# Performance work log

Hardware: AMD Instinct MI355X
Metric: run time of the kernel (lower is better)

## Reference

```python
import jax, jax.numpy as jnp
import numpy as np

IMAGE_SIZE = 224
BLUR_SIGMA = 4.0  # PIL ImageFilter.GaussianBlur(radius=4): radius acts as std dev
BLUR_RADIUS = 8   # truncate kernel at 2*sigma


def _gaussian_blur(x, sigma=BLUR_SIGMA, radius=BLUR_RADIUS):
    # separable gaussian blur on NCHW, SAME padding
    t = jnp.arange(-radius, radius + 1, dtype=x.dtype)
    kern = jnp.exp(-0.5 * (t / sigma) ** 2)
    kern = kern / kern.sum()
    dn = ('NCHW', 'OIHW', 'NCHW')
    x = jax.lax.conv_general_dilated(x, kern.reshape(1, 1, 1, -1), (1, 1), 'SAME', dimension_numbers=dn)
    x = jax.lax.conv_general_dilated(x, kern.reshape(1, 1, -1, 1), (1, 1), 'SAME', dimension_numbers=dn)
    return x


def setup_inputs() -> dict:
    key = jax.random.key(0)
    ks = jax.random.split(key, 8)
    N = 1000
    inp = {
        'z': jax.random.normal(ks[0], (1, 512), jnp.float32),
        'fmap0': jax.random.normal(ks[1], (1, 64, 56, 56), jnp.float32),
        'fmap1': jax.random.normal(ks[2], (1, 128, 28, 28), jnp.float32),
        'fmap2': jax.random.normal(ks[3], (1, 256, 14, 14), jnp.float32),
        'z_lib': jax.random.normal(ks[4], (N, 512), jnp.float32),
        'lib0': jax.random.normal(ks[5], (N, 64, 56, 56), jnp.float32),
        'lib1': jax.random.normal(ks[6], (N, 128, 28, 28), jnp.float32),
        'lib2': jax.random.normal(ks[7], (N, 256, 14, 14), jnp.float32),
        'k': 5,
    }
    return inp


def reference(z, fmap0, fmap1, fmap2, z_lib, lib0, lib1, lib2, k):
    # distances = ||z_lib - z||_2 over feature dim -> [N]
    dists = jnp.linalg.norm(z_lib - z, axis=1)
    # topk smallest
    neg_vals, indices = jax.lax.top_k(-dists, k)
    z_score = (-neg_vals).mean()

    s_total = jnp.zeros((1, 1, IMAGE_SIZE, IMAGE_SIZE), jnp.float32)
    for fmap, lib in ((fmap0, lib0), (fmap1, lib1), (fmap2, lib2)):
        nearest = lib[indices]                            # [k, C, H, W]
        s = jnp.linalg.norm(nearest - fmap, axis=1)        # [k, H, W] (channel-wise L2)
        s = s.min(axis=0, keepdims=True)                   # [1, H, W]
        s_up = jax.image.resize(s[None], (1, 1, IMAGE_SIZE, IMAGE_SIZE), method='bilinear')
        s_total = s_total + s_up
    s_total = _gaussian_blur(s_total)
    return z_score, s_total
```

## Files before the change

kernel.cpp:

```cpp
#include <hip/hip_runtime.h>
#include <hip/hip_bf16.h>
#include <math.h>

#define IMG 224
#define NLIB 1000
#define ZD 512
#define MAXK 8
#define NTHR 512
#define STHR 256


__device__ __forceinline__ int clampk(int k) {
    if (k < 1) k = 1;
    if (k > MAXK) k = MAXK;
    return k;
}

__global__ void __launch_bounds__(NTHR) k_dist(const float* __restrict__ z,
                                               const float* __restrict__ zlib,
                                               float* __restrict__ dists) {
    int lane = threadIdx.x & 63, wave = threadIdx.x >> 6;
    int gw = blockIdx.x * (NTHR / 64) + wave;
    if (gw >= NLIB) return;
    const float4* row4 = (const float4*)(zlib + (size_t)gw * ZD);
    const float4* z4   = (const float4*)z;
    float4 a0 = row4[lane],      b0 = z4[lane];
    float4 a1 = row4[64 + lane], b1 = z4[64 + lane];
    float acc = 0.f, d;
    d = a0.x - b0.x; acc += d * d;  d = a0.y - b0.y; acc += d * d;
    d = a0.z - b0.z; acc += d * d;  d = a0.w - b0.w; acc += d * d;
    d = a1.x - b1.x; acc += d * d;  d = a1.y - b1.y; acc += d * d;
    d = a1.z - b1.z; acc += d * d;  d = a1.w - b1.w; acc += d * d;
#pragma unroll
    for (int off = 32; off > 0; off >>= 1) acc += __shfl_xor(acc, off, 64);
    if (lane == 0) dists[gw] = sqrtf(acc);
}

__global__ void __launch_bounds__(STHR) k_score(
        const float* __restrict__ f0, const float* __restrict__ f1,
        const float* __restrict__ f2,
        const float* __restrict__ l0, const float* __restrict__ l1,
        const float* __restrict__ l2,
        const float* __restrict__ dists, const int* __restrict__ kp,
        float* __restrict__ out,
        float* __restrict__ s0, float* __restrict__ s1, float* __restrict__ s2) {

    int tid = threadIdx.x;
    int lane = tid & 63, wave = tid >> 6;
    int k = clampk(*kp);

    int n0 = k * 1568, n1 = k * 784, n2 = k * 392;
    int njobs = n0 + n1 + n2;
    int j = blockIdx.x * STHR + tid;

    const float* fmp = nullptr; const float* lbp = nullptr; float* op = nullptr;
    int kk = 0, pq = 0, cbase = 0, HW = 0, Cfull = 0;
    bool valid = (j < njobs);
    if (valid) {
        if (j < n0) {
            int r = j;           kk = r / 1568; int q = r % 1568;
            int part = q / 784;  pq = q % 784;  cbase = part * 32;
            HW = 3136; Cfull = 64;  fmp = f0; lbp = l0;
            op = s0 + part * (MAXK * 3136) + kk * 3136;
        } else if (j < n0 + n1) {
            int r = j - n0;      kk = r / 784;  int q = r % 784;
            int part = q / 196;  pq = q % 196;  cbase = part * 32;
            HW = 784;  Cfull = 128; fmp = f1; lbp = l1;
            op = s1 + part * (MAXK * 784) + kk * 784;
        } else {
            int r = j - n0 - n1; kk = r / 392;  int q = r % 392;
            int part = q / 49;   pq = q % 49;   cbase = part * 32;
            HW = 196;  Cfull = 256; fmp = f2; lbp = l2;
            op = s2 + part * (MAXK * 196) + kk * 196;
        }
    }

    int waveBase = blockIdx.x * STHR + wave * 64;
    bool dotopk = (waveBase < njobs) || (blockIdx.x == 0 && wave == 0);
    int myidx = 0;
    if (dotopk) {
        float vals[16];
#pragma unroll
        for (int q = 0; q < 16; ++q) {
            int e = lane + 64 * q;
            vals[q] = (e < NLIB) ? dists[e] : 3.4e38f;
        }
        float ssum = 0.f;
        for (int it = 0; it < k; ++it) {
            float bv = 3.4e38f; int bi = 0x7fffffff;
#pragma unroll
            for (int q = 0; q < 16; ++q) {
                if (vals[q] < bv) { bv = vals[q]; bi = lane + 64 * q; }
            }
#pragma unroll
            for (int off = 1; off < 64; off <<= 1) {
                float ov = __shfl_xor(bv, off, 64);
                int   oi = __shfl_xor(bi, off, 64);
                if (ov < bv || (ov == bv && oi < bi)) { bv = ov; bi = oi; }
            }
#pragma unroll
            for (int q = 0; q < 16; ++q) {
                if (lane + 64 * q == bi) vals[q] = 3.4e38f;
            }
            if (it == kk) myidx = bi;
            ssum += bv;
        }
        if (blockIdx.x == 0 && tid == 0) out[0] = ssum / (float)k;
    }

    if (!valid) return;

    const float4* lb4 = (const float4*)(lbp + (size_t)myidx * (size_t)Cfull * HW
                                            + (size_t)cbase * HW);
    const float4* fb4 = (const float4*)(fmp + (size_t)cbase * HW);
    int HW4 = HW >> 2;
    float ax = 0.f, ay = 0.f, az = 0.f, aw = 0.f;
#pragma unroll
    for (int c = 0; c < 32; ++c) {
        float4 a = lb4[c * HW4 + pq];
        float4 b = fb4[c * HW4 + pq];
        float dx = a.x - b.x, dy = a.y - b.y, dz = a.z - b.z, dw = a.w - b.w;
        ax += dx * dx; ay += dy * dy; az += dz * dz; aw += dw * dw;
    }
    float4 r; r.x = ax; r.y = ay; r.z = az; r.w = aw;
    ((float4*)op)[pq] = r;
}

__device__ __forceinline__ float bilin(const float* __restrict__ msm, int Wl, int Win,
                                       int bx, int by, float scl, int gx, int gy) {
    float sxf = ((float)gx + 0.5f) * scl - 0.5f;
    float syf = ((float)gy + 0.5f) * scl - 0.5f;
    float fx = floorf(sxf), fy = floorf(syf);
    float wx = sxf - fx,    wy = syf - fy;
    int ix = (int)fx, iy = (int)fy;
    int x0c = min(max(ix, 0), Win - 1) - bx, x1c = min(max(ix + 1, 0), Win - 1) - bx;
    int y0c = min(max(iy, 0), Win - 1) - by, y1c = min(max(iy + 1, 0), Win - 1) - by;
    float v00 = msm[y0c * Wl + x0c], v10 = msm[y0c * Wl + x1c];
    float v01 = msm[y1c * Wl + x0c], v11 = msm[y1c * Wl + x1c];
    return (1.f - wy) * ((1.f - wx) * v00 + wx * v10) +
           wy * ((1.f - wx) * v01 + wx * v11);
}

__global__ void __launch_bounds__(NTHR) k_tile(
        const float* __restrict__ s0, const float* __restrict__ s1,
        const float* __restrict__ s2, const int* __restrict__ kp,
        float* __restrict__ out) {

    __shared__ float msm0[100];
    __shared__ float msm1[36];
    __shared__ float msm2[9];
    __shared__ float pre[32 * 32];
    __shared__ float mid[32 * 16];
    __shared__ float wk[17];

    int tid = threadIdx.x;
    int k = clampk(*kp);
    int tx = blockIdx.x % 14, ty = blockIdx.x / 14;
    int x0 = tx * 16, y0 = ty * 16;
    int b0x = x0 / 4 - 3,  b0y = y0 / 4 - 3;
    int b1x = x0 / 8 - 2,  b1y = y0 / 8 - 2;
    int b2x = x0 / 16 - 1, b2y = y0 / 16 - 1;

    if (tid < 17) {
        float r = (float)(tid - 8) * 0.25f;
        wk[tid] = expf(-0.5f * r * r);
    }

    if (tid >= 64 && tid < 64 + 145) {
        int i = tid - 64;
        float m = 3.4e38f;
        if (i < 100) {
            int ly = i / 10, lx = i % 10;
            int gx = min(max(b0x + lx, 0), 55), gy = min(max(b0y + ly, 0), 55);
            int p = gy * 56 + gx;
            for (int kk = 0; kk < k; ++kk) {
                float v = s0[kk * 3136 + p] + s0[MAXK * 3136 + kk * 3136 + p];
                m = fminf(m, v);
            }
            msm0[i] = sqrtf(m);
        } else if (i < 136) {
            int r = i - 100; int ly = r / 6, lx = r % 6;
            int gx = min(max(b1x + lx, 0), 27), gy = min(max(b1y + ly, 0), 27);
            int p = gy * 28 + gx;
            for (int kk = 0; kk < k; ++kk) {
                float v = 0.f;
#pragma unroll
                for (int part = 0; part < 4; ++part)
                    v += s1[part * (MAXK * 784) + kk * 784 + p];
                m = fminf(m, v);
            }
            msm1[r] = sqrtf(m);
        } else {
            int r = i - 136; int ly = r / 3, lx = r % 3;
            int gx = min(max(b2x + lx, 0), 13), gy = min(max(b2y + ly, 0), 13);
            int p = gy * 14 + gx;
            for (int kk = 0; kk < k; ++kk) {
                float v = 0.f;
#pragma unroll
                for (int part = 0; part < 8; ++part)
                    v += s2[part * (MAXK * 196) + kk * 196 + p];
                m = fminf(m, v);
            }
            msm2[r] = sqrtf(m);
        }
    }
    __syncthreads();

    float wsum = 0.f;
#pragma unroll
    for (int t = 0; t < 17; ++t) wsum += wk[t];
    float inv2 = 1.f / (wsum * wsum);

    for (int i = tid; i < 32 * 32; i += NTHR) {
        int lx = i % 32, ly = i / 32;
        int gx = x0 - 8 + lx, gy = y0 - 8 + ly;
        float v = 0.f;
        if ((unsigned)gx < (unsigned)IMG && (unsigned)gy < (unsigned)IMG) {
            v = bilin(msm0, 10, 56, b0x, b0y, 0.25f,   gx, gy)
              + bilin(msm1, 6,  28, b1x, b1y, 0.125f,  gx, gy)
              + bilin(msm2, 3,  14, b2x, b2y, 0.0625f, gx, gy);
        }
        pre[i] = v;
    }
    __syncthreads();

    if (tid < 32 * 16) {
        int cx = tid % 16, ly = tid / 16;
        float acc = 0.f;
#pragma unroll
        for (int t = 0; t < 17; ++t) acc += wk[t] * pre[ly * 32 + cx + t];
        mid[ly * 16 + cx] = acc;
    }
    __syncthreads();

    if (tid < 16 * 16) {
        int ox = tid % 16, oy = tid / 16;
        float acc = 0.f;
#pragma unroll
        for (int t = 0; t < 17; ++t) acc += wk[t] * mid[(oy + t) * 16 + ox];
        out[1 + (y0 + oy) * IMG + (x0 + ox)] = acc * inv2;
    }
}

extern "C" void kernel_launch(void* const* d_in, const int* in_sizes, int n_in,
                              void* d_out, int out_size, void* d_ws, size_t ws_size,
                              hipStream_t stream) {
    const float* z    = (const float*)d_in[0];
    const float* f0   = (const float*)d_in[1];
    const float* f1   = (const float*)d_in[2];
    const float* f2   = (const float*)d_in[3];
    const float* zlib = (const float*)d_in[4];
    const float* l0   = (const float*)d_in[5];
    const float* l1   = (const float*)d_in[6];
    const float* l2   = (const float*)d_in[7];
    const int*   kp   = (const int*)d_in[8];
    float* out = (float*)d_out;

    float* ws    = (float*)d_ws;
    float* dists = ws;
    float* s0    = ws + 1024;
    float* s1    = s0 + 2 * MAXK * 3136;
    float* s2    = s1 + 4 * MAXK * 784;

    k_dist<<<(NLIB + 7) / 8, NTHR, 0, stream>>>(z, zlib, dists);

    int njobs = MAXK * (1568 + 784 + 392);
    k_score<<<(njobs + STHR - 1) / STHR, STHR, 0, stream>>>(
        f0, f1, f2, l0, l1, l2, dists, kp, out, s0, s1, s2);

    k_tile<<<196, NTHR, 0, stream>>>(s0, s1, s2, kp, out);
}
```

Baseline: 25.57 us.

## Fuse three kernels into one persistent kernel with grid-wide software barriers

Merges the distance, score and tile/blur kernels into a single 196-block launch, using flag-based grid barriers built on agent-scope atomics instead of kernel boundaries. Intermediate buffers are written and read with relaxed atomic stores and loads so results are visible across blocks. This removes two kernel launch gaps. The price is spin-wait barrier overhead and a reliance on all 196 blocks being co-resident. The barrier resets flags with relaxed ordering and has a timeout guard, so correctness across repeated calls depends on careful flag handling.

```diff
diff --git a/kernel.cpp b/kernel.cpp
--- a/kernel.cpp
+++ b/kernel.cpp
@@ -7,7 +7,8 @@
 #define ZD 512
 #define MAXK 8
 #define NTHR 512
-#define STHR 256
+#define NBLK 196
+#define MTAG 0x5EEDF00Du
 
 
 __device__ __forceinline__ int clampk(int k) {
@@ -16,42 +17,108 @@
     return k;
 }
 
-__global__ void __launch_bounds__(NTHR) k_dist(const float* __restrict__ z,
-                                               const float* __restrict__ zlib,
-                                               float* __restrict__ dists) {
-    int lane = threadIdx.x & 63, wave = threadIdx.x >> 6;
-    int gw = blockIdx.x * (NTHR / 64) + wave;
-    if (gw >= NLIB) return;
-    const float4* row4 = (const float4*)(zlib + (size_t)gw * ZD);
-    const float4* z4   = (const float4*)z;
-    float4 a0 = row4[lane],      b0 = z4[lane];
-    float4 a1 = row4[64 + lane], b1 = z4[64 + lane];
-    float acc = 0.f, d;
-    d = a0.x - b0.x; acc += d * d;  d = a0.y - b0.y; acc += d * d;
-    d = a0.z - b0.z; acc += d * d;  d = a0.w - b0.w; acc += d * d;
-    d = a1.x - b1.x; acc += d * d;  d = a1.y - b1.y; acc += d * d;
-    d = a1.z - b1.z; acc += d * d;  d = a1.w - b1.w; acc += d * d;
-#pragma unroll
-    for (int off = 32; off > 0; off >>= 1) acc += __shfl_xor(acc, off, 64);
-    if (lane == 0) dists[gw] = sqrtf(acc);
-}
-
-__global__ void __launch_bounds__(STHR) k_score(
+__device__ __forceinline__ void cgs_u32(unsigned* p, unsigned v) {
+    __hip_atomic_store(p, v, __ATOMIC_RELAXED, __HIP_MEMORY_SCOPE_AGENT);
+}
+__device__ __forceinline__ unsigned cgl_u32(unsigned* p) {
+    return __hip_atomic_load(p, __ATOMIC_RELAXED, __HIP_MEMORY_SCOPE_AGENT);
+}
+__device__ __forceinline__ void cgs_f32(float* p, float v) {
+    __hip_atomic_store(p, v, __ATOMIC_RELAXED, __HIP_MEMORY_SCOPE_AGENT);
+}
+__device__ __forceinline__ float cgl_f32(const float* p) {
+    return __hip_atomic_load((float*)p, __ATOMIC_RELAXED, __HIP_MEMORY_SCOPE_AGENT);
+}
+
+__device__ __forceinline__ void barrier_ar(unsigned* slots, int bid, int tid) {
+    __syncthreads();
+    if (tid == 0) cgs_u32(slots + bid, MTAG);
+    if (tid < 64) {
+        unsigned pend = 0;
+#pragma unroll
+        for (int q = 0; q < 4; ++q) { int i = q * 64 + tid; if (i < NBLK) pend |= 1u << q; }
+        long guard = 0;
+        for (;;) {
+#pragma unroll
+            for (int q = 0; q < 4; ++q) {
+                int i = q * 64 + tid;
+                if (pend & (1u << q))
+                    if (cgl_u32(slots + i) == MTAG) pend &= ~(1u << q);
+            }
+            if (__all(pend == 0)) break;
+            if (++guard > 100000000L) break;
+            __builtin_amdgcn_s_sleep(4);
+        }
+    }
+    __syncthreads();
+    asm volatile("" ::: "memory");
+}
+
+__device__ __forceinline__ float bilin(const float* __restrict__ msm, int Wl, int Win,
+                                       int bx, int by, float scl, int gx, int gy) {
+    float sxf = ((float)gx + 0.5f) * scl - 0.5f;
+    float syf = ((float)gy + 0.5f) * scl - 0.5f;
+    float fx = floorf(sxf), fy = floorf(syf);
+    float wx = sxf - fx,    wy = syf - fy;
+    int ix = (int)fx, iy = (int)fy;
+    int x0c = min(max(ix, 0), Win - 1) - bx, x1c = min(max(ix + 1, 0), Win - 1) - bx;
+    int y0c = min(max(iy, 0), Win - 1) - by, y1c = min(max(iy + 1, 0), Win - 1) - by;
+    float v00 = msm[y0c * Wl + x0c], v10 = msm[y0c * Wl + x1c];
+    float v01 = msm[y1c * Wl + x0c], v11 = msm[y1c * Wl + x1c];
+    return (1.f - wy) * ((1.f - wx) * v00 + wx * v10) +
+           wy * ((1.f - wx) * v01 + wx * v11);
+}
+
+__global__ void __launch_bounds__(NTHR) k_fused(
+        const float* __restrict__ z,
         const float* __restrict__ f0, const float* __restrict__ f1,
         const float* __restrict__ f2,
+        const float* __restrict__ zlib,
         const float* __restrict__ l0, const float* __restrict__ l1,
         const float* __restrict__ l2,
-        const float* __restrict__ dists, const int* __restrict__ kp,
+        const int* __restrict__ kp,
         float* __restrict__ out,
+        float* __restrict__ dists, unsigned* __restrict__ a1, unsigned* __restrict__ a2,
         float* __restrict__ s0, float* __restrict__ s1, float* __restrict__ s2) {
 
+    __shared__ float msm0[100], msm1[36], msm2[9];
+    __shared__ float pre[32 * 32];
+    __shared__ float mid[32 * 16];
+    __shared__ float wk[17];
+
     int tid = threadIdx.x;
+    int bid = blockIdx.x;
     int lane = tid & 63, wave = tid >> 6;
     int k = clampk(*kp);
 
+    if (bid == 0 && tid < NBLK) cgs_u32(a2 + tid, 0u);
+
+    if (tid < 17) {
+        float r = (float)(tid - 8) * 0.25f;
+        wk[tid] = expf(-0.5f * r * r);
+    }
+
+    int gw = bid * 8 + wave;
+    if (bid < 125 && gw < NLIB) {
+        const float4* row4 = (const float4*)(zlib + (size_t)gw * ZD);
+        const float4* z4   = (const float4*)z;
+        float4 a0 = row4[lane],      b0 = z4[lane];
+        float4 a1v = row4[64 + lane], b1v = z4[64 + lane];
+        float acc = 0.f, d;
+        d = a0.x - b0.x; acc += d * d;  d = a0.y - b0.y; acc += d * d;
+        d = a0.z - b0.z; acc += d * d;  d = a0.w - b0.w; acc += d * d;
+        d = a1v.x - b1v.x; acc += d * d;  d = a1v.y - b1v.y; acc += d * d;
+        d = a1v.z - b1v.z; acc += d * d;  d = a1v.w - b1v.w; acc += d * d;
+#pragma unroll
+        for (int off = 32; off > 0; off >>= 1) acc += __shfl_xor(acc, off, 64);
+        if (lane == 0) cgs_f32(&dists[gw], sqrtf(acc));
+    }
+
+    barrier_ar(a1, bid, tid);
+
     int n0 = k * 1568, n1 = k * 784, n2 = k * 392;
     int njobs = n0 + n1 + n2;
-    int j = blockIdx.x * STHR + tid;
+    int j = bid * NTHR + tid;
 
     const float* fmp = nullptr; const float* lbp = nullptr; float* op = nullptr;
     int kk = 0, pq = 0, cbase = 0, HW = 0, Cfull = 0;
@@ -75,15 +142,15 @@
         }
     }
 
-    int waveBase = blockIdx.x * STHR + wave * 64;
-    bool dotopk = (waveBase < njobs) || (blockIdx.x == 0 && wave == 0);
+    int waveBase = bid * NTHR + wave * 64;
+    bool dotopk = (waveBase < njobs) || (bid == 0 && wave == 0);
     int myidx = 0;
     if (dotopk) {
         float vals[16];
 #pragma unroll
         for (int q = 0; q < 16; ++q) {
             int e = lane + 64 * q;
-            vals[q] = (e < NLIB) ? dists[e] : 3.4e38f;
+            vals[q] = (e < NLIB) ? cgl_f32(&dists[e]) : 3.4e38f;
         }
         float ssum = 0.f;
         for (int it = 0; it < k; ++it) {
@@ -105,66 +172,36 @@
             if (it == kk) myidx = bi;
             ssum += bv;
         }
-        if (blockIdx.x == 0 && tid == 0) out[0] = ssum / (float)k;
-    }
-
-    if (!valid) return;
-
-    const float4* lb4 = (const float4*)(lbp + (size_t)myidx * (size_t)Cfull * HW
-                                            + (size_t)cbase * HW);
-    const float4* fb4 = (const float4*)(fmp + (size_t)cbase * HW);
-    int HW4 = HW >> 2;
-    float ax = 0.f, ay = 0.f, az = 0.f, aw = 0.f;
-#pragma unroll
-    for (int c = 0; c < 32; ++c) {
-        float4 a = lb4[c * HW4 + pq];
-        float4 b = fb4[c * HW4 + pq];
-        float dx = a.x - b.x, dy = a.y - b.y, dz = a.z - b.z, dw = a.w - b.w;
-        ax += dx * dx; ay += dy * dy; az += dz * dz; aw += dw * dw;
-    }
-    float4 r; r.x = ax; r.y = ay; r.z = az; r.w = aw;
-    ((float4*)op)[pq] = r;
-}
-
-__device__ __forceinline__ float bilin(const float* __restrict__ msm, int Wl, int Win,
-                                       int bx, int by, float scl, int gx, int gy) {
-    float sxf = ((float)gx + 0.5f) * scl - 0.5f;
-    float syf = ((float)gy + 0.5f) * scl - 0.5f;
-    float fx = floorf(sxf), fy = floorf(syf);
-    float wx = sxf - fx,    wy = syf - fy;
-    int ix = (int)fx, iy = (int)fy;
-    int x0c = min(max(ix, 0), Win - 1) - bx, x1c = min(max(ix + 1, 0), Win - 1) - bx;
-    int y0c = min(max(iy, 0), Win - 1) - by, y1c = min(max(iy + 1, 0), Win - 1) - by;
-    float v00 = msm[y0c * Wl + x0c], v10 = msm[y0c * Wl + x1c];
-    float v01 = msm[y1c * Wl + x0c], v11 = msm[y1c * Wl + x1c];
-    return (1.f - wy) * ((1.f - wx) * v00 + wx * v10) +
-           wy * ((1.f - wx) * v01 + wx * v11);
-}
-
-__global__ void __launch_bounds__(NTHR) k_tile(
-        const float* __restrict__ s0, const float* __restrict__ s1,
-        const float* __restrict__ s2, const int* __restrict__ kp,
-        float* __restrict__ out) {
-
-    __shared__ float msm0[100];
-    __shared__ float msm1[36];
-    __shared__ float msm2[9];
-    __shared__ float pre[32 * 32];
-    __shared__ float mid[32 * 16];
-    __shared__ float wk[17];
-
-    int tid = threadIdx.x;
-    int k = clampk(*kp);
-    int tx = blockIdx.x % 14, ty = blockIdx.x / 14;
+        if (bid == 0 && tid == 0) out[0] = ssum / (float)k;
+    }
+
+    if (valid) {
+        const float4* lb4 = (const float4*)(lbp + (size_t)myidx * (size_t)Cfull * HW
+                                                + (size_t)cbase * HW);
+        const float4* fb4 = (const float4*)(fmp + (size_t)cbase * HW);
+        int HW4 = HW >> 2;
+        float ax = 0.f, ay = 0.f, az = 0.f, aw = 0.f;
+#pragma unroll
+        for (int c = 0; c < 32; ++c) {
+            float4 a = lb4[c * HW4 + pq];
+            float4 b = fb4[c * HW4 + pq];
+            float dx = a.x - b.x, dy = a.y - b.y, dz = a.z - b.z, dw = a.w - b.w;
+            ax += dx * dx; ay += dy * dy; az += dz * dz; aw += dw * dw;
+        }
+        float* o = op + 4 * pq;
+        cgs_f32(o + 0, ax); cgs_f32(o + 1, ay);
+        cgs_f32(o + 2, az); cgs_f32(o + 3, aw);
+    }
+
+    barrier_ar(a2, bid, tid);
+
+    if (tid == 0) cgs_u32(a1 + bid, 0u);
+
+    int tx = bid % 14, ty = bid / 14;
     int x0 = tx * 16, y0 = ty * 16;
     int b0x = x0 / 4 - 3,  b0y = y0 / 4 - 3;
     int b1x = x0 / 8 - 2,  b1y = y0 / 8 - 2;
     int b2x = x0 / 16 - 1, b2y = y0 / 16 - 1;
-
-    if (tid < 17) {
-        float r = (float)(tid - 8) * 0.25f;
-        wk[tid] = expf(-0.5f * r * r);
-    }
 
     if (tid >= 64 && tid < 64 + 145) {
         int i = tid - 64;
@@ -173,8 +210,9 @@
             int ly = i / 10, lx = i % 10;
             int gx = min(max(b0x + lx, 0), 55), gy = min(max(b0y + ly, 0), 55);
             int p = gy * 56 + gx;
-            for (int kk = 0; kk < k; ++kk) {
-                float v = s0[kk * 3136 + p] + s0[MAXK * 3136 + kk * 3136 + p];
+            for (int kq = 0; kq < k; ++kq) {
+                float v = cgl_f32(&s0[kq * 3136 + p])
+                        + cgl_f32(&s0[MAXK * 3136 + kq * 3136 + p]);
                 m = fminf(m, v);
             }
             msm0[i] = sqrtf(m);
@@ -182,11 +220,11 @@
             int r = i - 100; int ly = r / 6, lx = r % 6;
             int gx = min(max(b1x + lx, 0), 27), gy = min(max(b1y + ly, 0), 27);
             int p = gy * 28 + gx;
-            for (int kk = 0; kk < k; ++kk) {
+            for (int kq = 0; kq < k; ++kq) {
                 float v = 0.f;
 #pragma unroll
                 for (int part = 0; part < 4; ++part)
-                    v += s1[part * (MAXK * 784) + kk * 784 + p];
+                    v += cgl_f32(&s1[part * (MAXK * 784) + kq * 784 + p]);
                 m = fminf(m, v);
             }
             msm1[r] = sqrtf(m);
@@ -194,11 +232,11 @@
             int r = i - 136; int ly = r / 3, lx = r % 3;
             int gx = min(max(b2x + lx, 0), 13), gy = min(max(b2y + ly, 0), 13);
             int p = gy * 14 + gx;
-            for (int kk = 0; kk < k; ++kk) {
+            for (int kq = 0; kq < k; ++kq) {
                 float v = 0.f;
 #pragma unroll
                 for (int part = 0; part < 8; ++part)
-                    v += s2[part * (MAXK * 196) + kk * 196 + p];
+                    v += cgl_f32(&s2[part * (MAXK * 196) + kq * 196 + p]);
                 m = fminf(m, v);
             }
             msm2[r] = sqrtf(m);
@@ -256,17 +294,14 @@
     const int*   kp   = (const int*)d_in[8];
     float* out = (float*)d_out;
 
-    float* ws    = (float*)d_ws;
-    float* dists = ws;
-    float* s0    = ws + 1024;
-    float* s1    = s0 + 2 * MAXK * 3136;
-    float* s2    = s1 + 4 * MAXK * 784;
-
-    k_dist<<<(NLIB + 7) / 8, NTHR, 0, stream>>>(z, zlib, dists);
-
-    int njobs = MAXK * (1568 + 784 + 392);
-    k_score<<<(njobs + STHR - 1) / STHR, STHR, 0, stream>>>(
-        f0, f1, f2, l0, l1, l2, dists, kp, out, s0, s1, s2);
-
-    k_tile<<<196, NTHR, 0, stream>>>(s0, s1, s2, kp, out);
-}
+    float*    ws    = (float*)d_ws;
+    float*    dists = ws;
+    unsigned* a1    = (unsigned*)(ws + 1024);
+    unsigned* a2    = (unsigned*)(ws + 1280);
+    float*    s0    = ws + 1536;
+    float*    s1    = s0 + 2 * MAXK * 3136;
+    float*    s2    = s1 + 4 * MAXK * 784;
+
+    k_fused<<<NBLK, NTHR, 0, stream>>>(z, f0, f1, f2, zlib, l0, l1, l2, kp,
+                                       out, dists, a1, a2, s0, s1, s2);
+}
```

After: 26.95 us. 1.05x slower.
